# Kernel optimization log

Measured on AMD Instinct MI355X. Metric: run time of the kernel, lower is better.

Reference implementation:

```python
import jax, jax.numpy as jnp
import numpy as np

N_SPECIAL = 4
LABEL_ID = 3
C_ACT = 64
C_TIME = 32
ACT_START = N_SPECIAL
TIME_START = N_SPECIAL + C_ACT
VOCAB = TIME_START + C_TIME  # 100
B, T, D = 8, 2048, 256


def l2norm(x, eps=1e-12):
    n = jnp.sqrt(jnp.sum(x * x, axis=-1, keepdims=True))
    return x / jnp.maximum(n, eps)


def causal_proto(h_norm, is_label, nxt, lo, hi, E_cls, alpha):
    """At every <LABEL> position L, build per-class prototypes from earlier
    support label positions (class = next token at that position), add a
    Bayesian prior alpha*E_cls, and return cosine sims of h_norm[L] vs protos.
    Non-label positions (or labels with no earlier support) -> zeros.
    Implemented as a single causal scan over time (online running sums)."""
    Bv, Tv, Dv = h_norm.shape
    C = E_cls.shape[0]
    is_sup = is_label & (nxt >= lo) & (nxt < hi)          # [B,T]
    cls = jnp.clip(nxt - lo, 0, C - 1)                    # [B,T]

    def step(carry, xs):
        Hsum, cnt = carry                                  # [B,C,D], [B,C]
        h_t, cls_t, sup_t, lab_t = xs                      # [B,D],[B],[B],[B]
        proto = l2norm((Hsum + alpha * E_cls) / (cnt[:, :, None] + alpha + 1e-8))
        sims = jnp.einsum('bd,bcd->bc', h_t, proto)        # cosine (h_t is unit)
        valid = lab_t & (jnp.sum(cnt, axis=-1) > 0)        # any earlier support
        out = jnp.where(valid[:, None], sims, 0.0)
        oh = jax.nn.one_hot(cls_t, C, dtype=h_t.dtype) * sup_t[:, None].astype(h_t.dtype)
        Hsum = Hsum + oh[:, :, None] * h_t[:, None, :]
        cnt = cnt + oh
        return (Hsum, cnt), out

    init = (jnp.zeros((Bv, C, Dv), h_norm.dtype), jnp.zeros((Bv, C), h_norm.dtype))
    xs = (jnp.swapaxes(h_norm, 0, 1), jnp.swapaxes(cls, 0, 1),
          jnp.swapaxes(is_sup, 0, 1), jnp.swapaxes(is_label, 0, 1))
    _, outs = jax.lax.scan(jax.checkpoint(step), init, xs)
    return jnp.swapaxes(outs, 0, 1)                        # [B,T,C]


def setup_inputs() -> dict:
    key = jax.random.key(0)
    ks = jax.random.split(key, 6)
    f32 = jnp.float32
    return {
        'tokens': jax.random.randint(ks[0], (B, T), 0, VOCAB, dtype=jnp.int32),
        'h': jax.random.normal(ks[1], (B, T, D), dtype=f32),
        'E': jax.random.normal(ks[2], (VOCAB, D), dtype=f32) * 0.02,
        'W_next': jax.random.normal(ks[3], (C_ACT, D), dtype=f32) * 0.02,
        'b_next': jnp.zeros((C_ACT,), f32),
        'W_time': jax.random.normal(ks[4], (C_TIME, D), dtype=f32) * 0.02,
        'b_time': jnp.zeros((C_TIME,), f32),
        'tied_scale_act': jnp.array(0.0, f32),
        'tied_scale_time': jnp.array(0.0, f32),
        'proto_scale_act': jnp.array(1.0, f32),
        'proto_scale_time': jnp.array(1.0, f32),
        'proto_prior_act': jnp.array(0.5, f32),
        'proto_prior_time': jnp.array(0.5, f32),
        'proto_temp_act': jnp.array(1.0, f32),
        'proto_temp_time': jnp.array(1.0, f32),
    }


def reference(tokens, h, E, W_next, b_next, W_time, b_time,
              tied_scale_act, tied_scale_time, proto_scale_act, proto_scale_time,
              proto_prior_act, proto_prior_time, proto_temp_act, proto_temp_time):
    sp = jax.nn.softplus
    # parametric heads
    param_next = jnp.einsum('btd,cd->btc', h, W_next) + b_next
    param_time = jnp.einsum('btd,cd->btc', h, W_time) + b_time
    # weight-tied heads (gradient flows into E here)
    tied_act = jnp.einsum('btd,cd->btc', h, E[ACT_START:TIME_START])
    tied_time = jnp.einsum('btd,cd->btc', h, E[TIME_START:VOCAB])
    # prototype head (E detached, as in the torch code)
    h_norm = l2norm(h)
    E_det = jax.lax.stop_gradient(E)
    E_act = l2norm(E_det[ACT_START:TIME_START])
    E_time = l2norm(E_det[TIME_START:VOCAB])
    nxt = jnp.roll(tokens, -1, axis=1)
    is_label = tokens == LABEL_ID
    proto_act = causal_proto(h_norm, is_label, nxt, ACT_START, TIME_START,
                             E_act, sp(proto_prior_act)) * sp(proto_temp_act)
    proto_time = causal_proto(h_norm, is_label, nxt, TIME_START, VOCAB,
                              E_time, sp(proto_prior_time)) * sp(proto_temp_time)
    activity_logits = param_next + sp(tied_scale_act) * tied_act + sp(proto_scale_act) * proto_act
    time_logits = param_time + sp(tied_scale_time) * tied_time + sp(proto_scale_time) * proto_time
    return (activity_logits, time_logits)
```

## Files before the change

kernel.cpp:

```cpp
#include <hip/hip_runtime.h>
#include <hip/hip_bf16.h>

#define Bv 8
#define Tv 2048
#define Dv 256
#define C_ACT 64
#define C_TIME 32
#define NCLS 96
#define LABEL_ID 3
#define ACT_START 4
#define TIME_START 68
#define VOCAB 100
#define MAXEV 36

typedef short bf16x8 __attribute__((ext_vector_type(8)));
typedef float f32x4  __attribute__((ext_vector_type(4)));

__device__ __forceinline__ float bf2f(__hip_bfloat16 x) { return __bfloat162float(x); }
__device__ __forceinline__ float bfb(unsigned short u) {
    union { unsigned int i; float f; } x; x.i = ((unsigned int)u) << 16; return x.f;
}
__device__ __forceinline__ short f2bs(float x) {
    __hip_bfloat16 b = __float2bfloat16(x);
    return *reinterpret_cast<short*>(&b);
}
__device__ __forceinline__ float spf(float x) { return log1pf(expf(x)); }

__device__ __forceinline__ float ldx(const void* p, size_t i, bool f32) {
    return f32 ? ((const float*)p)[i] : bf2f(((const __hip_bfloat16*)p)[i]);
}
__device__ __forceinline__ void stx(void* p, size_t i, float v, bool f32) {
    if (f32) ((float*)p)[i] = v;
    else     ((__hip_bfloat16*)p)[i] = __float2bfloat16(v);
}
__device__ __forceinline__ float4 ld4(const void* p, size_t i, bool f32) {
    if (f32) return *reinterpret_cast<const float4*>((const float*)p + i);
    ushort4 s = *reinterpret_cast<const ushort4*>((const unsigned short*)p + i);
    float4 u; u.x = bfb(s.x); u.y = bfb(s.y); u.z = bfb(s.z); u.w = bfb(s.w);
    return u;
}

__device__ __forceinline__ bool detect_f32_256(const void* h, int tid, int* s_cnt)
{
    if (tid == 0) *s_cnt = 0;
    __syncthreads();
    ushort4 u = *(reinterpret_cast<const ushort4*>(h) + tid);
    int c = 0; float v;
    v = bfb(u.x); if (!(fabsf(v) < 1e20f)) c++;
    v = bfb(u.y); if (!(fabsf(v) < 1e20f)) c++;
    v = bfb(u.z); if (!(fabsf(v) < 1e20f)) c++;
    v = bfb(u.w); if (!(fabsf(v) < 1e20f)) c++;
    #pragma unroll
    for (int o = 32; o > 0; o >>= 1) c += __shfl_down(c, o);
    if ((tid & 63) == 0 && c) atomicAdd(s_cnt, c);
    __syncthreads();
    return *s_cnt >= 4;
}

__device__ __forceinline__ size_t out_idx(int b, int L, int c)
{
    return (c < C_ACT)
        ? ((size_t)(b * Tv + L) * C_ACT + c)
        : ((size_t)Bv * Tv * C_ACT + (size_t)(b * Tv + L) * C_TIME + (c - C_ACT));
}

#define K1_ROWS 32
#define HPAD 72
#define EVLD 264
#define GLD 44

__global__ __launch_bounds__(256) void k_all(
    const int* __restrict__ tokens,
    const void* __restrict__ h,
    const void* __restrict__ E,
    const void* __restrict__ Wn, const void* __restrict__ bn,
    const void* __restrict__ Wt, const void* __restrict__ bt,
    const void* ts_a, const void* ts_t,
    const void* ps_a, const void* ps_t,
    const void* pp_a, const void* pp_t,
    const void* pt_a, const void* pt_t,
    void* __restrict__ out)
{
    __shared__ union {
        struct { short hB[K1_ROWS * HPAD]; short mB[NCLS * HPAD]; } t;
        struct {
            unsigned short hb[48][EVLD];
            union {
                unsigned short AsMs[48][EVLD];
                struct {
                    float Gl[MAXEV][GLD];
                    float P[MAXEV][24];
                    float Pm[MAXEV][24];
                    float SG[MAXEV][24];
                    float ZP[MAXEV][24];
                } r;
            } u2;
            float nrm[MAXEV];
        } s;
    } u;
    __shared__ int s_pos[MAXEV], s_cls[MAXEV];
    __shared__ unsigned long long s_mask[32];
    __shared__ unsigned long long s_mact, s_mtim;
    __shared__ int s_cnt, s_evn;

    int tid = threadIdx.x;
    bool f32 = detect_f32_256(h, tid, &s_cnt);
    float spt_a = spf(ldx(ts_a, 0, f32));
    float spt_t = spf(ldx(ts_t, 0, f32));

    if (blockIdx.x >= 32) {
        int R0   = (blockIdx.x - 32) * K1_ROWS;
        int w    = tid >> 6;
        int lane = tid & 63;
        int lr   = lane & 15;
        int quad = lane >> 4;
        int rt   = w & 1;
        int cg   = w >> 1;

        f32x4 acc[3];
        #pragma unroll
        for (int n = 0; n < 3; ++n) acc[n] = (f32x4){0.f, 0.f, 0.f, 0.f};

        for (int dc = 0; dc < 4; ++dc) {
            #pragma unroll
            for (int k = 0; k < 2; ++k) {
                int f = tid + k * 256;
                int row = f >> 4, dd4 = f & 15;
                float4 v = ld4(h, (size_t)(R0 + row) * Dv + dc * 64 + dd4 * 4, f32);
                short4 s4 = make_short4(f2bs(v.x), f2bs(v.y), f2bs(v.z), f2bs(v.w));
                *reinterpret_cast<short4*>(&u.t.hB[row * HPAD + dd4 * 4]) = s4;
            }
            #pragma unroll
            for (int k = 0; k < 6; ++k) {
                int f = tid + k * 256;
                int c = f >> 4, dd4 = f & 15;
                int col = dc * 64 + dd4 * 4;
                bool act = c < C_ACT;
                size_t wrow = act ? (size_t)c : (size_t)(c - C_ACT);
                int erow = act ? (ACT_START + c) : (TIME_START + (c - C_ACT));
                float4 w4 = ld4(act ? Wn : Wt, wrow * Dv + col, f32);
                float4 e4 = ld4(E, (size_t)erow * Dv + col, f32);
                float spt = act ? spt_a : spt_t;
                short4 s4 = make_short4(f2bs(w4.x + spt * e4.x),
                                        f2bs(w4.y + spt * e4.y),
                                        f2bs(w4.z + spt * e4.z),
                                        f2bs(w4.w + spt * e4.w));
                *reinterpret_cast<short4*>(&u.t.mB[c * HPAD + dd4 * 4]) = s4;
            }
            __syncthreads();

            #pragma unroll
            for (int ks = 0; ks < 2; ++ks) {
                int k0 = ks * 32;
                bf16x8 a = *reinterpret_cast<const bf16x8*>(
                    &u.t.hB[(16 * rt + lr) * HPAD + k0 + quad * 8]);
                #pragma unroll
                for (int nn = 0; nn < 3; ++nn) {
                    int n = 3 * cg + nn;
                    bf16x8 bfv = *reinterpret_cast<const bf16x8*>(
                        &u.t.mB[(16 * n + lr) * HPAD + k0 + quad * 8]);
                    acc[nn] = __builtin_amdgcn_mfma_f32_16x16x32_bf16(a, bfv, acc[nn], 0, 0, 0);
                }
            }
            __syncthreads();
        }

        #pragma unroll
        for (int nn = 0; nn < 3; ++nn) {
            int c = 16 * (3 * cg + nn) + lr;
            float bias = (c < C_ACT) ? ldx(bn, c, f32) : ldx(bt, c - C_ACT, f32);
            #pragma unroll
            for (int r = 0; r < 4; ++r) {
                int row = R0 + 16 * rt + quad * 4 + r;
                if (tokens[row] == LABEL_ID) continue;
                stx(out, out_idx(row >> 11, row & (Tv - 1), c), acc[nn][r] + bias, f32);
            }
        }
        return;
    }

    int b  = blockIdx.x >> 2;
    int q  = blockIdx.x & 3;
    int c0 = q * 24;
    int lane = tid & 63, wvx = tid >> 6;
    int lr = lane & 15, quad = lane >> 4;
    (void)lr; (void)quad;

    int* s_tok = reinterpret_cast<int*>(&u.s.u2.AsMs[0][0]);
    #pragma unroll
    for (int k = 0; k < 8; ++k) {
        int i = tid + 256 * k;
        int tok = tokens[(size_t)b * Tv + i];
        s_tok[i] = tok;
        unsigned long long m = __ballot(tok == LABEL_ID);
        if (lane == 0) s_mask[wvx + 4 * k] = m;
    }
    __syncthreads();

    if (wvx == 0) {
        unsigned long long m = (lane < 32) ? s_mask[lane] : 0ull;
        int cnt = __popcll(m);
        int x = cnt;
        #pragma unroll
        for (int d = 1; d < 32; d <<= 1) {
            int src = lane - d;
            int y = __shfl(x, src < 0 ? 0 : src);
            if (lane >= d) x += y;
        }
        if (lane < 32) {
            int n = x - cnt;
            unsigned long long mm = m;
            while (mm && n < MAXEV) {
                int bit = __builtin_ctzll(mm);
                s_pos[n++] = lane * 64 + bit;
                mm &= mm - 1;
            }
        }
        if (lane == 31) s_evn = (x < MAXEV) ? x : MAXEV;
    }
    __syncthreads();
    int evn = s_evn;
    int nrt = (evn + 15) >> 4;

    if (tid < evn) {
        int nxt = s_tok[(s_pos[tid] + 1) & (Tv - 1)];
        int c = -1;
        if (nxt >= ACT_START && nxt < TIME_START)  c = nxt - ACT_START;
        else if (nxt >= TIME_START && nxt < VOCAB) c = C_ACT + (nxt - TIME_START);
        s_cls[tid] = c;
    }

    {
        float4 hv[9];
        #pragma unroll
        for (int k = 0; k < 9; ++k) {
            int i = wvx + 4 * k;
            if (i < evn)
                hv[k] = ld4(h, ((size_t)b * Tv + s_pos[i]) * Dv + lane * 4, f32);
        }
        #pragma unroll
        for (int k = 0; k < 9; ++k) {
            int i = wvx + 4 * k;
            if (i < evn) {
                float4 v = hv[k];
                float p = v.x * v.x + v.y * v.y + v.z * v.z + v.w * v.w;
                #pragma unroll
                for (int o = 32; o > 0; o >>= 1) p += __shfl_xor(p, o);
                float nr = fmaxf(sqrtf(p), 1e-12f);
                float inv = 1.0f / nr;
                ushort4 s4;
                s4.x = (unsigned short)f2bs(v.x * inv);
                s4.y = (unsigned short)f2bs(v.y * inv);
                s4.z = (unsigned short)f2bs(v.z * inv);
                s4.w = (unsigned short)f2bs(v.w * inv);
                *reinterpret_cast<ushort4*>(&u.s.hb[i][lane * 4]) = s4;
                if (lane == 0) u.s.nrm[i] = nr;
            }
        }
        for (int i = evn + wvx; i < 16 * nrt; i += 4) {
            ushort4 z; z.x = z.y = z.z = z.w = 0;
            *reinterpret_cast<ushort4*>(&u.s.hb[i][lane * 4]) = z;
        }
    }
    __syncthreads();

    float alpha_a = spf(ldx(pp_a, 0, f32));
    float alpha_t = spf(ldx(pp_t, 0, f32));

    {
        float4 ev[6], wv6[6];
        #pragma unroll
        for (int k = 0; k < 6; ++k) {
            int lc = wvx + 4 * k, c = c0 + lc;
            bool act = c < C_ACT;
            int erow = act ? (ACT_START + c) : (TIME_START + (c - C_ACT));
            size_t wrow = act ? (size_t)c : (size_t)(c - C_ACT);
            ev[k]  = ld4(E, (size_t)erow * Dv + lane * 4, f32);
            wv6[k] = ld4(act ? Wn : Wt, wrow * Dv + lane * 4, f32);
        }
        #pragma unroll
        for (int k = 0; k < 6; ++k) {
            int lc = wvx + 4 * k, c = c0 + lc;
            bool act = c < C_ACT;
            float4 e4 = ev[k], w4 = wv6[k];
            float p = e4.x * e4.x + e4.y * e4.y + e4.z * e4.z + e4.w * e4.w;
            #pragma unroll
            for (int o = 32; o > 0; o >>= 1) p += __shfl_xor(p, o);
            float alpha = act ? alpha_a : alpha_t;
            float ai  = alpha / fmaxf(sqrtf(p), 1e-12f);
            float spt = act ? spt_a : spt_t;
            ushort4 a4, m4;
            a4.x = (unsigned short)f2bs(e4.x * ai);
            a4.y = (unsigned short)f2bs(e4.y * ai);
            a4.z = (unsigned short)f2bs(e4.z * ai);
            a4.w = (unsigned short)f2bs(e4.w * ai);
            m4.x = (unsigned short)f2bs(w4.x + spt * e4.x);
            m4.y = (unsigned short)f2bs(w4.y + spt * e4.y);
            m4.z = (unsigned short)f2bs(w4.z + spt * e4.z);
            m4.w = (unsigned short)f2bs(w4.w + spt * e4.w);
            *reinterpret_cast<ushort4*>(&u.s.u2.AsMs[lc][lane * 4])      = a4;
            *reinterpret_cast<ushort4*>(&u.s.u2.AsMs[24 + lc][lane * 4]) = m4;
        }
    }
    __syncthreads();

    {
        int lr2 = lane & 15, quad2 = lane >> 4;
        int nct = 3 + nrt;
        int TT  = nrt * nct;
        f32x4 accs[5];
        #pragma unroll
        for (int kk = 0; kk < 5; ++kk) {
            int t = wvx + 4 * kk;
            if (t < TT) {
                int rt2 = t / nct, ct = t - rt2 * nct;
                int ar = 16 * rt2 + lr2;
                const unsigned short* bbase = (ct < 3)
                    ? &u.s.u2.AsMs[16 * ct + lr2][0]
                    : &u.s.hb[16 * (ct - 3) + lr2][0];
                f32x4 acc = (f32x4){0.f, 0.f, 0.f, 0.f};
                #pragma unroll
                for (int ks = 0; ks < 8; ++ks) {
                    bf16x8 a  = *reinterpret_cast<const bf16x8*>(
                        &u.s.hb[ar][ks * 32 + quad2 * 8]);
                    bf16x8 bf = *reinterpret_cast<const bf16x8*>(
                        &bbase[ks * 32 + quad2 * 8]);
                    acc = __builtin_amdgcn_mfma_f32_16x16x32_bf16(a, bf, acc, 0, 0, 0);
                }
                accs[kk] = acc;
            }
        }
        __syncthreads();
        #pragma unroll
        for (int kk = 0; kk < 5; ++kk) {
            int t = wvx + 4 * kk;
            if (t < TT) {
                int rt2 = t / nct, ct = t - rt2 * nct;
                #pragma unroll
                for (int r = 0; r < 4; ++r) {
                    int row = 16 * rt2 + quad2 * 4 + r;
                    if (row >= evn) continue;
                    if (ct < 3) {
                        int cc = 16 * ct + lr2;
                        if (cc < 24) u.s.u2.r.P[row][cc] = accs[kk][r];
                        else         u.s.u2.r.Pm[row][cc - 24] = accs[kk][r];
                    } else {
                        int j = 16 * (ct - 3) + lr2;
                        if (j < evn) u.s.u2.r.Gl[row][j] = accs[kk][r];
                    }
                }
            }
        }
    }
    __syncthreads();

    for (int t = tid; t < evn * 24; t += 256) {
        int i = t / 24, lc = t - i * 24;
        int c = c0 + lc;
        float s = 0.f;
        #pragma unroll 4
        for (int j = 0; j < i; ++j)
            s += (s_cls[j] == c) ? u.s.u2.r.Gl[i][j] : 0.f;
        u.s.u2.r.SG[i][lc] = s;
    }
    if (wvx == 1) {
        int cj = (lane < evn) ? s_cls[lane] : -1;
        unsigned long long ma = __ballot(cj >= 0 && cj < C_ACT);
        unsigned long long mt = __ballot(cj >= C_ACT);
        if (lane == 0) { s_mact = ma; s_mtim = mt; }
    }
    __syncthreads();

    {
        int j = lane;
        float gjj = 0.f; int cj = -1;
        if (j < evn) { gjj = u.s.u2.r.Gl[j][j]; cj = s_cls[j]; }
        #pragma unroll
        for (int t6 = 0; t6 < 6; ++t6) {
            int lc = wvx * 6 + t6;
            int c = c0 + lc;
            float z = 0.f;
            if (j < evn && cj == c)
                z = 2.f * (u.s.u2.r.P[j][lc] + u.s.u2.r.SG[j][lc]) + gjj;
            float x = z;
            #pragma unroll
            for (int d = 1; d < 64; d <<= 1) {
                int src = lane - d;
                float y = __shfl(x, src < 0 ? 0 : src);
                if (lane >= d) x += y;
            }
            if (j < evn) u.s.u2.r.ZP[j][lc] = x - z;
        }
    }
    __syncthreads();

    {
        float mult_a = spf(ldx(ps_a, 0, f32)) * spf(ldx(pt_a, 0, f32));
        float mult_t = spf(ldx(ps_t, 0, f32)) * spf(ldx(pt_t, 0, f32));
        unsigned long long ma = s_mact, mt = s_mtim;
        for (int t = tid; t < evn * 24; t += 256) {
            int i = t / 24, lc = t - i * 24;
            int c = c0 + lc;
            bool actc = c < C_ACT;
            float alpha = actc ? alpha_a : alpha_t;
            float bias  = actc ? ldx(bn, c, f32) : ldx(bt, c - C_ACT, f32);
            float mult  = actc ? mult_a : mult_t;
            unsigned long long m = actc ? ma : mt;
            bool any = (m & ((1ull << i) - 1ull)) != 0ull;
            float v = u.s.u2.r.Pm[i][lc] * u.s.nrm[i] + bias;
            if (any) {
                float num = u.s.u2.r.P[i][lc] + u.s.u2.r.SG[i][lc];
                float n2  = alpha * alpha + u.s.u2.r.ZP[i][lc];
                v += mult * (num / fmaxf(sqrtf(n2), 1e-20f));
            }
            stx(out, out_idx(b, s_pos[i], c), v, f32);
        }
    }
}

extern "C" void kernel_launch(void* const* d_in, const int* in_sizes, int n_in,
                              void* d_out, int out_size, void* d_ws, size_t ws_size,
                              hipStream_t stream)
{
    const int* tokens = (const int*)d_in[0];
    const void* h    = d_in[1];
    const void* E    = d_in[2];
    const void* Wn   = d_in[3];
    const void* bn   = d_in[4];
    const void* Wt   = d_in[5];
    const void* bt   = d_in[6];
    const void* ts_a = d_in[7];
    const void* ts_t = d_in[8];
    const void* ps_a = d_in[9];
    const void* ps_t = d_in[10];
    const void* pp_a = d_in[11];
    const void* pp_t = d_in[12];
    const void* pt_a = d_in[13];
    const void* pt_t = d_in[14];

    k_all<<<32 + (Bv * Tv) / K1_ROWS, 256, 0, stream>>>(
        tokens, h, E, Wn, bn, Wt, bt,
        ts_a, ts_t, ps_a, ps_t, pp_a, pp_t, pt_a, pt_t, d_out);
}
```

Before: 115.3 us.

## Restructure GEMM blocks: full-K weight tile in LDS, A fragments from global

```diff
diff --git a/kernel.cpp b/kernel.cpp
--- a/kernel.cpp
+++ b/kernel.cpp
@@ -15,6 +15,7 @@
 
 typedef short bf16x8 __attribute__((ext_vector_type(8)));
 typedef float f32x4  __attribute__((ext_vector_type(4)));
+typedef unsigned short u16x8 __attribute__((ext_vector_type(8)));
 
 __device__ __forceinline__ float bf2f(__hip_bfloat16 x) { return __bfloat162float(x); }
 __device__ __forceinline__ float bfb(unsigned short u) {
@@ -64,8 +65,7 @@
         : ((size_t)Bv * Tv * C_ACT + (size_t)(b * Tv + L) * C_TIME + (c - C_ACT));
 }
 
-#define K1_ROWS 32
-#define HPAD 72
+#define K1_ROWS 64
 #define EVLD 264
 #define GLD 44
 
@@ -82,7 +82,7 @@
     void* __restrict__ out)
 {
     __shared__ union {
-        struct { short hB[K1_ROWS * HPAD]; short mB[NCLS * HPAD]; } t;
+        unsigned short mB[NCLS][EVLD];
         struct {
             unsigned short hb[48][EVLD];
             union {
@@ -114,66 +114,96 @@
         int lane = tid & 63;
         int lr   = lane & 15;
         int quad = lane >> 4;
-        int rt   = w & 1;
-        int cg   = w >> 1;
-
-        f32x4 acc[3];
-        #pragma unroll
-        for (int n = 0; n < 3; ++n) acc[n] = (f32x4){0.f, 0.f, 0.f, 0.f};
-
+
+        int rowb = 16 * w + quad * 4;
+        int tk[4]; float bs[6];
+        #pragma unroll
+        for (int r = 0; r < 4; ++r) tk[r] = tokens[R0 + rowb + r];
+        #pragma unroll
+        for (int n = 0; n < 6; ++n) {
+            int c = 16 * n + lr;
+            bs[n] = (c < C_ACT) ? ldx(bn, c, f32) : ldx(bt, c - C_ACT, f32);
+        }
+
+        #pragma unroll 4
+        for (int k = 0; k < 12; ++k) {
+            int f = tid + 256 * k;
+            int c = f >> 5, col = (f & 31) * 8;
+            bool act = c < C_ACT;
+            size_t wrow = act ? (size_t)c : (size_t)(c - C_ACT);
+            size_t erow = act ? (size_t)(ACT_START + c) : (size_t)(TIME_START + (c - C_ACT));
+            const void* wptr = act ? Wn : Wt;
+            float spt = act ? spt_a : spt_t;
+            float4 w0 = ld4(wptr, wrow * Dv + col,     f32);
+            float4 w1 = ld4(wptr, wrow * Dv + col + 4, f32);
+            float4 e0 = ld4(E,    erow * Dv + col,     f32);
+            float4 e1 = ld4(E,    erow * Dv + col + 4, f32);
+            u16x8 m8;
+            m8[0] = (unsigned short)f2bs(w0.x + spt * e0.x);
+            m8[1] = (unsigned short)f2bs(w0.y + spt * e0.y);
+            m8[2] = (unsigned short)f2bs(w0.z + spt * e0.z);
+            m8[3] = (unsigned short)f2bs(w0.w + spt * e0.w);
+            m8[4] = (unsigned short)f2bs(w1.x + spt * e1.x);
+            m8[5] = (unsigned short)f2bs(w1.y + spt * e1.y);
+            m8[6] = (unsigned short)f2bs(w1.z + spt * e1.z);
+            m8[7] = (unsigned short)f2bs(w1.w + spt * e1.w);
+            *reinterpret_cast<u16x8*>(&u.mB[c][col]) = m8;
+        }
+
+        bf16x8 av[8];
+        if (!f32) {
+            const unsigned short* aB = (const unsigned short*)h
+                + (size_t)(R0 + 16 * w + lr) * Dv + quad * 8;
+            #pragma unroll
+            for (int dc = 0; dc < 4; ++dc)
+                #pragma unroll
+                for (int ks = 0; ks < 2; ++ks)
+                    av[dc * 2 + ks] = *reinterpret_cast<const bf16x8*>(
+                        aB + dc * 64 + ks * 32);
+        } else {
+            const float* aB = (const float*)h
+                + (size_t)(R0 + 16 * w + lr) * Dv + quad * 8;
+            #pragma unroll
+            for (int dc = 0; dc < 4; ++dc)
+                #pragma unroll
+                for (int ks = 0; ks < 2; ++ks) {
+                    float4 a0 = *reinterpret_cast<const float4*>(aB + dc * 64 + ks * 32);
+                    float4 a1 = *reinterpret_cast<const float4*>(aB + dc * 64 + ks * 32 + 4);
+                    bf16x8 a;
+                    a[0] = f2bs(a0.x); a[1] = f2bs(a0.y); a[2] = f2bs(a0.z); a[3] = f2bs(a0.w);
+                    a[4] = f2bs(a1.x); a[5] = f2bs(a1.y); a[6] = f2bs(a1.z); a[7] = f2bs(a1.w);
+                    av[dc * 2 + ks] = a;
+                }
+        }
+
+        __syncthreads();
+
+        f32x4 acc[6];
+        #pragma unroll
+        for (int n = 0; n < 6; ++n) acc[n] = (f32x4){0.f, 0.f, 0.f, 0.f};
+        #pragma unroll
         for (int dc = 0; dc < 4; ++dc) {
             #pragma unroll
-            for (int k = 0; k < 2; ++k) {
-                int f = tid + k * 256;
-                int row = f >> 4, dd4 = f & 15;
-                float4 v = ld4(h, (size_t)(R0 + row) * Dv + dc * 64 + dd4 * 4, f32);
-                short4 s4 = make_short4(f2bs(v.x), f2bs(v.y), f2bs(v.z), f2bs(v.w));
-                *reinterpret_cast<short4*>(&u.t.hB[row * HPAD + dd4 * 4]) = s4;
-            }
-            #pragma unroll
-            for (int k = 0; k < 6; ++k) {
-                int f = tid + k * 256;
-                int c = f >> 4, dd4 = f & 15;
-                int col = dc * 64 + dd4 * 4;
-                bool act = c < C_ACT;
-                size_t wrow = act ? (size_t)c : (size_t)(c - C_ACT);
-                int erow = act ? (ACT_START + c) : (TIME_START + (c - C_ACT));
-                float4 w4 = ld4(act ? Wn : Wt, wrow * Dv + col, f32);
-                float4 e4 = ld4(E, (size_t)erow * Dv + col, f32);
-                float spt = act ? spt_a : spt_t;
-                short4 s4 = make_short4(f2bs(w4.x + spt * e4.x),
-                                        f2bs(w4.y + spt * e4.y),
-                                        f2bs(w4.z + spt * e4.z),
-                                        f2bs(w4.w + spt * e4.w));
-                *reinterpret_cast<short4*>(&u.t.mB[c * HPAD + dd4 * 4]) = s4;
-            }
-            __syncthreads();
-
-            #pragma unroll
             for (int ks = 0; ks < 2; ++ks) {
-                int k0 = ks * 32;
-                bf16x8 a = *reinterpret_cast<const bf16x8*>(
-                    &u.t.hB[(16 * rt + lr) * HPAD + k0 + quad * 8]);
-                #pragma unroll
-                for (int nn = 0; nn < 3; ++nn) {
-                    int n = 3 * cg + nn;
-                    bf16x8 bfv = *reinterpret_cast<const bf16x8*>(
-                        &u.t.mB[(16 * n + lr) * HPAD + k0 + quad * 8]);
-                    acc[nn] = __builtin_amdgcn_mfma_f32_16x16x32_bf16(a, bfv, acc[nn], 0, 0, 0);
+                bf16x8 a = av[dc * 2 + ks];
+                int koff = dc * 64 + ks * 32 + quad * 8;
+                #pragma unroll
+                for (int n = 0; n < 6; ++n) {
+                    bf16x8 b = *reinterpret_cast<const bf16x8*>(
+                        &u.mB[16 * n + lr][koff]);
+                    acc[n] = __builtin_amdgcn_mfma_f32_16x16x32_bf16(a, b, acc[n], 0, 0, 0);
                 }
             }
-            __syncthreads();
-        }
-
-        #pragma unroll
-        for (int nn = 0; nn < 3; ++nn) {
-            int c = 16 * (3 * cg + nn) + lr;
-            float bias = (c < C_ACT) ? ldx(bn, c, f32) : ldx(bt, c - C_ACT, f32);
+        }
+
+        #pragma unroll
+        for (int n = 0; n < 6; ++n) {
+            int c = 16 * n + lr;
             #pragma unroll
             for (int r = 0; r < 4; ++r) {
-                int row = R0 + 16 * rt + quad * 4 + r;
-                if (tokens[row] == LABEL_ID) continue;
-                stx(out, out_idx(row >> 11, row & (Tv - 1), c), acc[nn][r] + bias, f32);
+                if (tk[r] == LABEL_ID) continue;
+                int row = R0 + rowb + r;
+                stx(out, out_idx(row >> 11, row & (Tv - 1), c), acc[n][r] + bs[n], f32);
             }
         }
         return;
@@ -183,8 +213,6 @@
     int q  = blockIdx.x & 3;
     int c0 = q * 24;
     int lane = tid & 63, wvx = tid >> 6;
-    int lr = lane & 15, quad = lane >> 4;
-    (void)lr; (void)quad;
 
     int* s_tok = reinterpret_cast<int*>(&u.s.u2.AsMs[0][0]);
     #pragma unroll
```

Result: no change. 115.1 us (-0.2%).

## Load GEMM operands directly into registers, dropping LDS staging and syncs

Applied to the files above, without the earlier changes.

```diff
diff --git a/kernel.cpp b/kernel.cpp
--- a/kernel.cpp
+++ b/kernel.cpp
@@ -15,6 +15,7 @@
 
 typedef short bf16x8 __attribute__((ext_vector_type(8)));
 typedef float f32x4  __attribute__((ext_vector_type(4)));
+typedef unsigned short u16x8 __attribute__((ext_vector_type(8)));
 
 __device__ __forceinline__ float bf2f(__hip_bfloat16 x) { return __bfloat162float(x); }
 __device__ __forceinline__ float bfb(unsigned short u) {
@@ -64,8 +65,6 @@
         : ((size_t)Bv * Tv * C_ACT + (size_t)(b * Tv + L) * C_TIME + (c - C_ACT));
 }
 
-#define K1_ROWS 32
-#define HPAD 72
 #define EVLD 264
 #define GLD 44
 
@@ -82,7 +81,6 @@
     void* __restrict__ out)
 {
     __shared__ union {
-        struct { short hB[K1_ROWS * HPAD]; short mB[NCLS * HPAD]; } t;
         struct {
             unsigned short hb[48][EVLD];
             union {
@@ -109,72 +107,82 @@
     float spt_t = spf(ldx(ts_t, 0, f32));
 
     if (blockIdx.x >= 32) {
-        int R0   = (blockIdx.x - 32) * K1_ROWS;
+        int tb   = blockIdx.x - 32;
+        int rb   = tb / 6;
+        int cb   = tb - 6 * rb;
         int w    = tid >> 6;
         int lane = tid & 63;
         int lr   = lane & 15;
         int quad = lane >> 4;
-        int rt   = w & 1;
-        int cg   = w >> 1;
-
-        f32x4 acc[3];
-        #pragma unroll
-        for (int n = 0; n < 3; ++n) acc[n] = (f32x4){0.f, 0.f, 0.f, 0.f};
-
-        for (int dc = 0; dc < 4; ++dc) {
+
+        int arow = rb * 64 + 16 * w;
+        int c    = cb * 16 + lr;
+        bool act = cb < 4;
+        float spt = act ? spt_a : spt_t;
+
+        int tk[4];
+        #pragma unroll
+        for (int r = 0; r < 4; ++r) tk[r] = tokens[arow + quad * 4 + r];
+        float bias = act ? ldx(bn, c, f32) : ldx(bt, c - C_ACT, f32);
+
+        f32x4 acc = (f32x4){0.f, 0.f, 0.f, 0.f};
+
+        if (!f32) {
+            const unsigned short* aB = (const unsigned short*)h
+                + (size_t)(arow + lr) * Dv + quad * 8;
+            const unsigned short* wB = (act ? (const unsigned short*)Wn + (size_t)c * Dv
+                                            : (const unsigned short*)Wt + (size_t)(c - C_ACT) * Dv)
+                + quad * 8;
+            const unsigned short* eB = (const unsigned short*)E
+                + (size_t)(act ? (ACT_START + c) : (TIME_START + (c - C_ACT))) * Dv + quad * 8;
+
+            bf16x8 a8[8]; u16x8 w8[8], e8[8];
             #pragma unroll
-            for (int k = 0; k < 2; ++k) {
-                int f = tid + k * 256;
-                int row = f >> 4, dd4 = f & 15;
-                float4 v = ld4(h, (size_t)(R0 + row) * Dv + dc * 64 + dd4 * 4, f32);
-                short4 s4 = make_short4(f2bs(v.x), f2bs(v.y), f2bs(v.z), f2bs(v.w));
-                *reinterpret_cast<short4*>(&u.t.hB[row * HPAD + dd4 * 4]) = s4;
+            for (int t = 0; t < 8; ++t) {
+                int off = t * 32;
+                a8[t] = *reinterpret_cast<const bf16x8*>(aB + off);
+                w8[t] = *reinterpret_cast<const u16x8*>(wB + off);
+                e8[t] = *reinterpret_cast<const u16x8*>(eB + off);
             }
             #pragma unroll
-            for (int k = 0; k < 6; ++k) {
-                int f = tid + k * 256;
-                int c = f >> 4, dd4 = f & 15;
-                int col = dc * 64 + dd4 * 4;
-                bool act = c < C_ACT;
-                size_t wrow = act ? (size_t)c : (size_t)(c - C_ACT);
-                int erow = act ? (ACT_START + c) : (TIME_START + (c - C_ACT));
-                float4 w4 = ld4(act ? Wn : Wt, wrow * Dv + col, f32);
-                float4 e4 = ld4(E, (size_t)erow * Dv + col, f32);
-                float spt = act ? spt_a : spt_t;
-                short4 s4 = make_short4(f2bs(w4.x + spt * e4.x),
-                                        f2bs(w4.y + spt * e4.y),
-                                        f2bs(w4.z + spt * e4.z),
-                                        f2bs(w4.w + spt * e4.w));
-                *reinterpret_cast<short4*>(&u.t.mB[c * HPAD + dd4 * 4]) = s4;
-            }
-            __syncthreads();
-
+            for (int t = 0; t < 8; ++t) {
+                bf16x8 m;
+                #pragma unroll
+                for (int j = 0; j < 8; ++j)
+                    m[j] = f2bs(bfb(w8[t][j]) + spt * bfb(e8[t][j]));
+                acc = __builtin_amdgcn_mfma_f32_16x16x32_bf16(a8[t], m, acc, 0, 0, 0);
+            }
+        } else {
+            const float* aB = (const float*)h + (size_t)(arow + lr) * Dv + quad * 8;
+            const float* wB = (act ? (const float*)Wn + (size_t)c * Dv
+                                   : (const float*)Wt + (size_t)(c - C_ACT) * Dv) + quad * 8;
+            const float* eB = (const float*)E
+                + (size_t)(act ? (ACT_START + c) : (TIME_START + (c - C_ACT))) * Dv + quad * 8;
             #pragma unroll
-            for (int ks = 0; ks < 2; ++ks) {
-                int k0 = ks * 32;
-                bf16x8 a = *reinterpret_cast<const bf16x8*>(
-                    &u.t.hB[(16 * rt + lr) * HPAD + k0 + quad * 8]);
-                #pragma unroll
-                for (int nn = 0; nn < 3; ++nn) {
-                    int n = 3 * cg + nn;
-                    bf16x8 bfv = *reinterpret_cast<const bf16x8*>(
-                        &u.t.mB[(16 * n + lr) * HPAD + k0 + quad * 8]);
-                    acc[nn] = __builtin_amdgcn_mfma_f32_16x16x32_bf16(a, bfv, acc[nn], 0, 0, 0);
-                }
-            }
-            __syncthreads();
-        }
-
-        #pragma unroll
-        for (int nn = 0; nn < 3; ++nn) {
-            int c = 16 * (3 * cg + nn) + lr;
-            float bias = (c < C_ACT) ? ldx(bn, c, f32) : ldx(bt, c - C_ACT, f32);
-            #pragma unroll
-            for (int r = 0; r < 4; ++r) {
-                int row = R0 + 16 * rt + quad * 4 + r;
-                if (tokens[row] == LABEL_ID) continue;
-                stx(out, out_idx(row >> 11, row & (Tv - 1), c), acc[nn][r] + bias, f32);
-            }
+            for (int t = 0; t < 8; ++t) {
+                int off = t * 32;
+                float4 a0 = *reinterpret_cast<const float4*>(aB + off);
+                float4 a1 = *reinterpret_cast<const float4*>(aB + off + 4);
+                float4 w0 = *reinterpret_cast<const float4*>(wB + off);
+                float4 w1 = *reinterpret_cast<const float4*>(wB + off + 4);
+                float4 e0 = *reinterpret_cast<const float4*>(eB + off);
+                float4 e1 = *reinterpret_cast<const float4*>(eB + off + 4);
+                bf16x8 a, m;
+                a[0] = f2bs(a0.x); a[1] = f2bs(a0.y); a[2] = f2bs(a0.z); a[3] = f2bs(a0.w);
+                a[4] = f2bs(a1.x); a[5] = f2bs(a1.y); a[6] = f2bs(a1.z); a[7] = f2bs(a1.w);
+                m[0] = f2bs(w0.x + spt * e0.x); m[1] = f2bs(w0.y + spt * e0.y);
+                m[2] = f2bs(w0.z + spt * e0.z); m[3] = f2bs(w0.w + spt * e0.w);
+                m[4] = f2bs(w1.x + spt * e1.x); m[5] = f2bs(w1.y + spt * e1.y);
+                m[6] = f2bs(w1.z + spt * e1.z); m[7] = f2bs(w1.w + spt * e1.w);
+                acc = __builtin_amdgcn_mfma_f32_16x16x32_bf16(a, m, acc, 0, 0, 0);
+            }
+        }
+
+        #pragma unroll
+        for (int r = 0; r < 4; ++r) {
+            if (tk[r] == LABEL_ID) continue;
+            int row = arow + quad * 4 + r;
+            stx(out, out_idx(row >> 11, row & (Tv - 1), c), acc[r] + bias, f32);
         }
         return;
     }
@@ -183,8 +191,6 @@
     int q  = blockIdx.x & 3;
     int c0 = q * 24;
     int lane = tid & 63, wvx = tid >> 6;
-    int lr = lane & 15, quad = lane >> 4;
-    (void)lr; (void)quad;
 
     int* s_tok = reinterpret_cast<int*>(&u.s.u2.AsMs[0][0]);
     #pragma unroll
@@ -438,7 +444,7 @@
     const void* pt_a = d_in[13];
     const void* pt_t = d_in[14];
 
-    k_all<<<32 + (Bv * Tv) / K1_ROWS, 256, 0, stream>>>(
+    k_all<<<32 + 1536, 256, 0, stream>>>(
         tokens, h, E, Wn, bn, Wt, bt,
         ts_a, ts_t, ps_a, ps_t, pp_a, pp_t, pt_a, pt_t, d_out);
 }
```

After: 131.2 us. +13.7%, slower.
